# Kernel tuning notes

Measured on AMD Instinct MI355X. Metric: run time of the kernel, lower is better.

## Reference

```python
import jax, jax.numpy as jnp
import numpy as np

DIM = 1024
NUM_HEADS = 16
HEAD_DIM = DIM // NUM_HEADS
INNER_ITR = 4
INNER_LR = 1.0
SCALE_QKV = 1.0


def setup_inputs() -> dict:
    key = jax.random.key(0)
    k1, k2, k3 = jax.random.split(key, 3)
    B, N, C = 8, 1024, DIM
    x = jax.random.normal(k1, (B, N, C), dtype=jnp.float32)
    # Xavier-uniform-ish scaled dense kernels
    w_qkv = jax.random.normal(k2, (C, 3 * C), dtype=jnp.float32) * (1.0 / np.sqrt(C))
    w_proj = jax.random.normal(k3, (C, C), dtype=jnp.float32) * (1.0 / np.sqrt(C))
    b_proj = jnp.zeros((C,), dtype=jnp.float32)
    return {"x": x, "w_qkv": w_qkv, "w_proj": w_proj, "b_proj": b_proj, "training": 0}


def _mttt_base(q, k, v):
    """MTTT 'base' inner loop: per (B,H) linear model W,b trained by
    INNER_ITR full-batch GD steps on MSE reconstruction of v from k,
    then applied to q. Shapes: q,k,v are (B, H, N, d)."""
    B, H, N, d = q.shape
    W = jnp.zeros((B, H, d, d), dtype=q.dtype)
    b = jnp.zeros((B, H, 1, d), dtype=q.dtype)
    invN = 1.0 / N
    for _ in range(INNER_ITR):  # small fixed iteration count
        pred = jnp.einsum('bhnd,bhde->bhne', k, W) + b   # (B,H,N,d)
        err = pred - v
        gW = jnp.einsum('bhnd,bhne->bhde', k, err) * invN
        gb = jnp.mean(err, axis=2, keepdims=True)
        W = W - INNER_LR * gW
        b = b - INNER_LR * gb
    return jnp.einsum('bhnd,bhde->bhne', q, W) + b       # (B,H,N,d)


def reference(x, w_qkv, w_proj, b_proj, training):
    B, N, C = x.shape
    H, d = NUM_HEADS, HEAD_DIM
    qkv = jnp.einsum('bnc,ce->bne', x, w_qkv)            # (B,N,3C), qkv_bias=False
    qkv = qkv.reshape(B, N, 3, H, d).transpose(2, 0, 3, 1, 4)  # (3,B,H,N,d)
    qkv = qkv * SCALE_QKV
    q, k, v = qkv[0], qkv[1], qkv[2]
    # qk_norm=False -> identity; scale_q=False -> no q scaling
    out = _mttt_base(q, k, v)                            # (B,H,N,d)
    out = out.transpose(0, 2, 1, 3).reshape(B, N, C)
    out = jnp.einsum('bnc,cd->bnd', out, w_proj) + b_proj
    # proj dropout deterministic (training=False)
    return out
```

## Files before the change

### kernel.cpp

```cpp
#include <hip/hip_runtime.h>


#define SEQ    1024
#define NBATCH 8
#define DIMC   1024
#define NHEAD  16
#define HDIM   64
#define MROWS  8192
#define NQKV   3072

typedef __attribute__((ext_vector_type(8))) __bf16 bf16x8;
typedef __attribute__((ext_vector_type(4))) float  f32x4;

__device__ __forceinline__ unsigned short f2b(float f) {
  union { float f; unsigned int u; } v; v.f = f;
  unsigned int r = (v.u + 0x7FFFu + ((v.u >> 16) & 1u)) >> 16;
  return (unsigned short)r;
}

__device__ __forceinline__ void load_lds16(const void* g, void* l) {
  __builtin_amdgcn_global_load_lds(
      (__attribute__((address_space(1))) void*)(void*)(g),
      (__attribute__((address_space(3))) void*)(l), 16, 0, 0);
}

#define FENCE asm volatile("" ::: "memory")
#define BAR   __builtin_amdgcn_s_barrier()

__global__ __launch_bounds__(256) void prep(const float* __restrict__ x,
                                            const float* __restrict__ wq,
                                            const float* __restrict__ wp,
                                            unsigned short* __restrict__ xb,
                                            unsigned short* __restrict__ wqT,
                                            unsigned short* __restrict__ wpT) {
  __shared__ unsigned short tile[32][33];
  const int bid = blockIdx.x, tid = threadIdx.x;
  if (bid < 8192) {
    int i = bid * 256 + tid;
    float4 v = ((const float4*)x)[i];
    ushort4 o;
    o.x = f2b(v.x); o.y = f2b(v.y); o.z = f2b(v.z); o.w = f2b(v.w);
    ((ushort4*)xb)[i] = o;
    return;
  }
  const float* in; unsigned short* out; int R, Cc, tix;
  if (bid < 8192 + 3072) { tix = bid - 8192; in = wq; out = wqT; R = 1024; Cc = 3072; }
  else                   { tix = bid - 8192 - 3072; in = wp; out = wpT; R = 1024; Cc = 1024; }
  const int nbx = Cc / 32;
  const int c0 = (tix % nbx) * 32, r0 = (tix / nbx) * 32;
  const int tx = tid & 31, ty = tid >> 5;
  for (int i = ty; i < 32; i += 8)
    tile[i][tx] = f2b(in[(size_t)(r0 + i) * Cc + c0 + tx]);
  __syncthreads();
  for (int i = ty; i < 32; i += 8)
    out[(size_t)(c0 + i) * R + r0 + tx] = tile[tx][i];
}

template <int BM, int BN, int WM, int WN, int ASTRIDE, int BMODE, int PERB>
__device__ __forceinline__
void gemm_r3(const unsigned short* __restrict__ A,
             const unsigned short* __restrict__ BT,
             void* __restrict__ Cout,
             const float* __restrict__ bias,
             int N, int NBN) {
  constexpr int THREADS = WM * WN * 64;
  constexpr int MF      = BM / (WM * 16);
  constexpr int NF      = BN / (WN * 16);
  constexpr int TR      = THREADS / 4;
  constexpr int ABYTES  = BM * 64;
  constexpr int TBYTES  = (BM + BN) * 64;
  constexpr int CALLS   = TBYTES / (THREADS * 16);
  constexpr int NT      = 32;

  extern __shared__ __align__(16) char ldsb[];

  const int tid  = threadIdx.x;
  const int lane = tid & 63, wave = tid >> 6;
  const int wr = wave / WN, wc = wave % WN;
  const int frow = lane & 15, g4 = lane >> 4;
  const int cz = (g4 ^ ((frow >> 1) & 3)) * 16;

  const int cpx = gridDim.x >> 3;
  const int wg  = (blockIdx.x & 7) * cpx + (blockIdx.x >> 3);
  const int bm = wg / NBN, bn = wg % NBN;
  const size_t m0 = (size_t)bm * BM, n0 = (size_t)bn * BN;

  const unsigned short* BTb = PERB ? (BT + (m0 >> 10) * (size_t)(1024 * 1024)) : BT;

  const int trow = tid >> 2;
  const int scol = ((tid & 3) ^ ((tid >> 3) & 3)) * 8;
  const unsigned short* psrc[CALLS];
#pragma unroll
  for (int c = 0; c < CALLS; ++c) {
    const int rr = c * TR + trow;
    psrc[c] = (rr < BM) ? (A + (m0 + rr) * (size_t)ASTRIDE + scol)
                        : (BTb + (size_t)(n0 + rr - BM) * 1024 + scol);
  }

  f32x4 acc[MF][NF];
  if (BMODE == 2) {
    const float* bp = bias + (m0 >> 10) * (size_t)N;
#pragma unroll
    for (int j = 0; j < NF; ++j) {
      float4 bv = *(const float4*)&bp[n0 + wc * (BN / WN) + j * 16 + g4 * 4];
      f32x4 t; t[0] = bv.x; t[1] = bv.y; t[2] = bv.z; t[3] = bv.w;
#pragma unroll
      for (int i = 0; i < MF; ++i) acc[i][j] = t;
    }
  } else {
#pragma unroll
    for (int i = 0; i < MF; ++i)
#pragma unroll
      for (int j = 0; j < NF; ++j) acc[i][j] = f32x4{0.f, 0.f, 0.f, 0.f};
  }

  auto stage = [&](int tk, int buf) {
    char* base = ldsb + buf * TBYTES + wave * 1024;
#pragma unroll
    for (int c = 0; c < CALLS; ++c)
      load_lds16(psrc[c] + tk * 32, base + c * (THREADS * 16));
  };

  const int aoff = (wr * (BM / WM) + frow) * 64 + cz;
  const int boff = ABYTES + (wc * (BN / WN) + frow) * 64 + cz;

  stage(0, 0); stage(1, 1);
  asm volatile("s_waitcnt vmcnt(%0)" :: "i"(CALLS) : "memory");
  FENCE; BAR;

  int bcur = 0, bpre = 2;
#pragma unroll 1
  for (int t = 0; t < NT; ++t) {
    if (t + 2 < NT) stage(t + 2, bpre);
    const char* rb = ldsb + bcur * TBYTES;
    bf16x8 af[MF], bq[NF];
#pragma unroll
    for (int i = 0; i < MF; ++i) af[i] = *(const bf16x8*)(rb + aoff + i * 1024);
#pragma unroll
    for (int j = 0; j < NF; ++j) bq[j] = *(const bf16x8*)(rb + boff + j * 1024);
#pragma unroll
    for (int i = 0; i < MF; ++i)
#pragma unroll
      for (int j = 0; j < NF; ++j)
        acc[i][j] = __builtin_amdgcn_mfma_f32_16x16x32_bf16(bq[j], af[i],
                                                            acc[i][j], 0, 0, 0);
    if (t + 2 < NT) asm volatile("s_waitcnt vmcnt(%0)" :: "i"(CALLS) : "memory");
    else            asm volatile("s_waitcnt vmcnt(0)" ::: "memory");
    FENCE; BAR;
    bcur = (bcur == 2) ? 0 : bcur + 1;
    bpre = (bpre == 2) ? 0 : bpre + 1;
  }

  const size_t mbase = m0 + wr * (BM / WM) + frow;
  const size_t nbase = n0 + wc * (BN / WN) + g4 * 4;
  if (BMODE == 2) {
    float* C = (float*)Cout;
#pragma unroll
    for (int i = 0; i < MF; ++i)
#pragma unroll
      for (int j = 0; j < NF; ++j) {
        float4 o; o.x = acc[i][j][0]; o.y = acc[i][j][1];
        o.z = acc[i][j][2]; o.w = acc[i][j][3];
        *(float4*)&C[(mbase + i * 16) * N + nbase + j * 16] = o;
      }
  } else {
    unsigned short* C = (unsigned short*)Cout;
#pragma unroll
    for (int i = 0; i < MF; ++i)
#pragma unroll
      for (int j = 0; j < NF; ++j) {
        ushort4 o; o.x = f2b(acc[i][j][0]); o.y = f2b(acc[i][j][1]);
        o.z = f2b(acc[i][j][2]); o.w = f2b(acc[i][j][3]);
        *(ushort4*)&C[(mbase + i * 16) * N + nbase + j * 16] = o;
      }
  }
}

__global__ __launch_bounds__(512, 4) void g_qkv(const unsigned short* __restrict__ A,
                                                const unsigned short* __restrict__ BT,
                                                void* __restrict__ C,
                                                const float* __restrict__ bias, int N, int NBN) {
  gemm_r3<128, 256, 2, 4, 1024, 0, 0>(A, BT, C, bias, N, NBN);
}
__global__ __launch_bounds__(256, 3) void g_out(const unsigned short* __restrict__ A,
                                                const unsigned short* __restrict__ BT,
                                                void* __restrict__ C,
                                                const float* __restrict__ bias, int N, int NBN) {
  gemm_r3<128, 128, 2, 2, NQKV, 2, 1>(A, BT, C, bias, N, NBN);
}

__global__ __launch_bounds__(256) void stats_gd(const unsigned short* __restrict__ qkvb,
                                                unsigned short* __restrict__ Wfb,
                                                float* __restrict__ bvec) {
  __shared__ __align__(16) char smem[52224];
  unsigned short (*kd)[136] = (unsigned short(*)[136])(smem);
  unsigned short (*vd)[136] = (unsigned short(*)[136])(smem + 17408);
  unsigned short (*kn)[64]  = (unsigned short(*)[64])(smem + 34816);
  unsigned short (*vn)[64]  = (unsigned short(*)[64])(smem + 43008);
  float (*Gs)[68] = (float(*)[68])(smem);
  float (*Ps)[68] = (float(*)[68])(smem + 17408);
  float (*Ws)[68] = (float(*)[68])(smem + 34816);
  __shared__ float mks[64], mvs[64], bs[64];

  const int bh = blockIdx.x, b = bh >> 4, h = bh & 15;
  const int tid = threadIdx.x;
  const int lane = tid & 63, wave = tid >> 6;
  const int frow = lane & 15;
  const int fk = (lane >> 4) * 8;

  const unsigned short* kg = qkvb + (size_t)b * 1024 * 3072 + 1024 + h * 64;
  const unsigned short* vg = qkvb + (size_t)b * 1024 * 3072 + 2048 + h * 64;

  typedef __attribute__((ext_vector_type(8))) unsigned short u16x8;
  u16x8 onesu = {0x3F80, 0x3F80, 0x3F80, 0x3F80, 0x3F80, 0x3F80, 0x3F80, 0x3F80};
  const bf16x8 ones = __builtin_bit_cast(bf16x8, onesu);

  f32x4 accG[4], accP[4], accK1, accV1;
#pragma unroll
  for (int j = 0; j < 4; ++j) {
    accG[j] = f32x4{0.f, 0.f, 0.f, 0.f};
    accP[j] = f32x4{0.f, 0.f, 0.f, 0.f};
  }
  accK1 = f32x4{0.f, 0.f, 0.f, 0.f};
  accV1 = f32x4{0.f, 0.f, 0.f, 0.f};

  const size_t srcn = (size_t)(tid >> 3) * 3072 + (tid & 7) * 8;
  const int td = tid & 63, tng = tid >> 6;

  for (int ch = 0; ch < 16; ++ch) {
    const size_t nb0 = (size_t)ch * 64;
#pragma unroll
    for (int c = 0; c < 2; ++c) {
      load_lds16(kg + (nb0 + 32 * c) * 3072 + srcn, (char*)kn + c * 4096 + wave * 1024);
      load_lds16(vg + (nb0 + 32 * c) * 3072 + srcn, (char*)vn + c * 4096 + wave * 1024);
    }
    asm volatile("s_waitcnt vmcnt(0)" ::: "memory");
    FENCE; BAR;
    {
      alignas(16) unsigned short pk[16], pv[16];
#pragma unroll
      for (int j = 0; j < 16; ++j) {
        pk[j] = kn[tng * 16 + j][td];
        pv[j] = vn[tng * 16 + j][td];
      }
      *(uint4*)&kd[td][tng * 16]     = *(const uint4*)pk;
      *(uint4*)&kd[td][tng * 16 + 8] = *(const uint4*)(pk + 8);
      *(uint4*)&vd[td][tng * 16]     = *(const uint4*)pv;
      *(uint4*)&vd[td][tng * 16 + 8] = *(const uint4*)(pv + 8);
    }
    FENCE; BAR;
#pragma unroll
    for (int ks = 0; ks < 2; ++ks) {
      const int nb = ks * 32 + fk;
      bf16x8 afk = *(const bf16x8*)&kd[wave * 16 + frow][nb];
      bf16x8 afv = *(const bf16x8*)&vd[wave * 16 + frow][nb];
      bf16x8 kf[4], vf[4];
#pragma unroll
      for (int j = 0; j < 4; ++j) {
        kf[j] = *(const bf16x8*)&kd[j * 16 + frow][nb];
        vf[j] = *(const bf16x8*)&vd[j * 16 + frow][nb];
      }
#pragma unroll
      for (int j = 0; j < 4; ++j) {
        accG[j] = __builtin_amdgcn_mfma_f32_16x16x32_bf16(afk, kf[j], accG[j], 0, 0, 0);
        accP[j] = __builtin_amdgcn_mfma_f32_16x16x32_bf16(afk, vf[j], accP[j], 0, 0, 0);
      }
      accK1 = __builtin_amdgcn_mfma_f32_16x16x32_bf16(afk, ones, accK1, 0, 0, 0);
      accV1 = __builtin_amdgcn_mfma_f32_16x16x32_bf16(afv, ones, accV1, 0, 0, 0);
    }
    FENCE; BAR;
  }

  const float invN = 1.0f / (float)SEQ;
  const int orow = wave * 16 + (lane >> 4) * 4;
#pragma unroll
  for (int j = 0; j < 4; ++j)
#pragma unroll
    for (int r = 0; r < 4; ++r) {
      Gs[orow + r][j * 16 + frow] = accG[j][r] * invN;
      Ps[orow + r][j * 16 + frow] = accP[j][r] * invN;
    }
  if (frow == 0) {
#pragma unroll
    for (int r = 0; r < 4; ++r) {
      mks[orow + r] = accK1[r] * invN;
      mvs[orow + r] = accV1[r] * invN;
    }
  }
  const int r = tid >> 2;
  const int c0 = (tid & 3) * 16;
  if (tid < 64) bs[tid] = 0.f;
#pragma unroll
  for (int c = 0; c < 16; ++c) Ws[r][c0 + c] = 0.f;
  __syncthreads();

  for (int it = 0; it < 4; ++it) {
    float wn[16];
#pragma unroll
    for (int c = 0; c < 16; ++c)
      wn[c] = Ws[r][c0 + c] + Ps[r][c0 + c] - mks[r] * bs[c0 + c];
    for (int j = 0; j < 64; ++j) {
      float g = Gs[r][j];
#pragma unroll
      for (int c = 0; c < 16; ++c) wn[c] -= g * Ws[j][c0 + c];
    }
    float bn = 0.f;
    if (tid < 64) {
      bn = mvs[tid];
      for (int j = 0; j < 64; ++j) bn -= mks[j] * Ws[j][tid];
    }
    __syncthreads();
#pragma unroll
    for (int c = 0; c < 16; ++c) Ws[r][c0 + c] = wn[c];
    if (tid < 64) bs[tid] = bn;
    __syncthreads();
  }

  unsigned short* wout = Wfb + (size_t)bh * HDIM * HDIM;
#pragma unroll
  for (int c = 0; c < 16; ++c)
    wout[(size_t)r * HDIM + c0 + c] = f2b(Ws[r][c0 + c]);
  if (tid < 64) bvec[(size_t)bh * HDIM + tid] = bs[tid];
}

__global__ __launch_bounds__(256) void wc_build(const unsigned short* __restrict__ wpT,
                                                const unsigned short* __restrict__ Wfb,
                                                unsigned short* __restrict__ WcT,
                                                const float* __restrict__ wp,
                                                const float* __restrict__ bvec,
                                                float* __restrict__ part) {
  const int tid = threadIdx.x;
  if (blockIdx.y == 4) {
    if (blockIdx.x >= 64) return;
    const int p  = (blockIdx.x & 3) * 256 + tid;
    const int cc = blockIdx.x >> 2;
    float s[8];
#pragma unroll
    for (int b = 0; b < 8; ++b) s[b] = 0.f;
    const int c0 = cc * 64;
    for (int c = c0; c < c0 + 64; ++c) {
      float w = wp[(size_t)c * 1024 + p];
#pragma unroll
      for (int b = 0; b < 8; ++b) s[b] += bvec[b * 1024 + c] * w;
    }
    float* dst = part + (size_t)cc * 8192;
#pragma unroll
    for (int b = 0; b < 8; ++b) dst[b * 1024 + p] = s[b];
    return;
  }
  const int bh = blockIdx.x;
  const int pblk = blockIdx.y;
  const int b = bh >> 4, h = bh & 15;
  const int lane = tid & 63, wave = tid >> 6;
  const int frow = lane & 15, g4 = lane >> 4, fk = g4 * 8;
  const int p0 = pblk * 256 + wave * 64;

  f32x4 acc[4][4];
#pragma unroll
  for (int i = 0; i < 4; ++i)
#pragma unroll
    for (int j = 0; j < 4; ++j) acc[i][j] = f32x4{0.f, 0.f, 0.f, 0.f};

  const unsigned short* wb = Wfb + (size_t)bh * 4096;
#pragma unroll
  for (int kk = 0; kk < 2; ++kk) {
    bf16x8 af[4], bq[4];
#pragma unroll
    for (int i = 0; i < 4; ++i)
      af[i] = *(const bf16x8*)&wpT[(size_t)(p0 + i * 16 + frow) * 1024 + h * 64 + kk * 32 + fk];
#pragma unroll
    for (int j = 0; j < 4; ++j)
      bq[j] = *(const bf16x8*)&wb[(size_t)(j * 16 + frow) * 64 + kk * 32 + fk];
#pragma unroll
    for (int i = 0; i < 4; ++i)
#pragma unroll
      for (int j = 0; j < 4; ++j)
        acc[i][j] = __builtin_amdgcn_mfma_f32_16x16x32_bf16(bq[j], af[i], acc[i][j], 0, 0, 0);
  }

  unsigned short* dst = WcT + (size_t)b * 1024 * 1024;
#pragma unroll
  for (int i = 0; i < 4; ++i)
#pragma unroll
    for (int j = 0; j < 4; ++j) {
      ushort4 o; o.x = f2b(acc[i][j][0]); o.y = f2b(acc[i][j][1]);
      o.z = f2b(acc[i][j][2]); o.w = f2b(acc[i][j][3]);
      *(ushort4*)&dst[(size_t)(p0 + i * 16 + frow) * 1024 + h * 64 + j * 16 + g4 * 4] = o;
    }
}

__global__ __launch_bounds__(256) void bc_reduce(const float* __restrict__ part,
                                                 const float* __restrict__ b_proj,
                                                 float* __restrict__ bc) {
  const int idx = blockIdx.x * 256 + threadIdx.x;
  const int p = idx & 1023;
  float s = b_proj[p];
#pragma unroll
  for (int cc = 0; cc < 16; ++cc) s += part[(size_t)cc * 8192 + idx];
  bc[idx] = s;
}

extern "C" void kernel_launch(void* const* d_in, const int* in_sizes, int n_in,
                              void* d_out, int out_size, void* d_ws, size_t ws_size,
                              hipStream_t stream) {
  const float* x      = (const float*)d_in[0];
  const float* w_qkv  = (const float*)d_in[1];
  const float* w_proj = (const float*)d_in[2];
  const float* b_proj = (const float*)d_in[3];

  char* ws = (char*)d_ws;
  unsigned short* xb    = (unsigned short*)(ws + 0);
  unsigned short* wqT   = (unsigned short*)(ws + 16777216);
  unsigned short* wpT   = (unsigned short*)(ws + 23068672);
  unsigned short* qkvb  = (unsigned short*)(ws + 25165824);
  unsigned short* WcT   = (unsigned short*)(ws + 109051904);
  unsigned short* Wfb   = (unsigned short*)(ws + 125829120);
  float*          bvec  = (float*)(ws + 126877696);
  float*          bc    = (float*)(ws + 126910464);
  float*          bpart = (float*)(ws + 126943232);
  if (ws_size < (size_t)127467520) return;

  hipFuncSetAttribute((const void*)g_qkv, hipFuncAttributeMaxDynamicSharedMemorySize, 73728);
  hipFuncSetAttribute((const void*)g_out, hipFuncAttributeMaxDynamicSharedMemorySize, 49152);

  prep<<<dim3(8192 + 3072 + 1024), 256, 0, stream>>>(x, w_qkv, w_proj, xb, wqT, wpT);
  g_qkv<<<dim3(768), dim3(512), 73728, stream>>>(xb, wqT, qkvb, nullptr, NQKV, 12);
  stats_gd<<<128, 256, 0, stream>>>(qkvb, Wfb, bvec);
  wc_build<<<dim3(128, 5), 256, 0, stream>>>(wpT, Wfb, WcT, w_proj, bvec, bpart);
  bc_reduce<<<32, 256, 0, stream>>>(bpart, b_proj, bc);
  g_out<<<dim3(512), dim3(256), 49152, stream>>>(qkvb, WcT, d_out, bc, DIMC, 8);
}
```

Measured before the change: 166.1 us.

## Split per-head statistics reduction across two blocks and add separate GD solve kernel

The fused stats+GD kernel, which ran only 128 blocks, is split in two. A statistics kernel now uses 256 blocks, each reducing half the sequence and writing raw MFMA accumulators to workspace that reuses the xb region. A new gd_solve kernel sums the two partials and runs the inner gradient-descent iterations. The aim is better CU occupancy during the memory-bound Gram-matrix pass, at the cost of one extra launch and a partial-sum round trip through global memory.

```diff
diff --git a/kernel.cpp b/kernel.cpp
--- a/kernel.cpp
+++ b/kernel.cpp
@@ -189,20 +189,17 @@
   gemm_r3<128, 128, 2, 2, NQKV, 2, 1>(A, BT, C, bias, N, NBN);
 }
 
-__global__ __launch_bounds__(256) void stats_gd(const unsigned short* __restrict__ qkvb,
-                                                unsigned short* __restrict__ Wfb,
-                                                float* __restrict__ bvec) {
-  __shared__ __align__(16) char smem[52224];
+__global__ __launch_bounds__(256) void stats_part(const unsigned short* __restrict__ qkvb,
+                                                  float* __restrict__ spart) {
+  __shared__ __align__(16) char smem[51200];
   unsigned short (*kd)[136] = (unsigned short(*)[136])(smem);
   unsigned short (*vd)[136] = (unsigned short(*)[136])(smem + 17408);
   unsigned short (*kn)[64]  = (unsigned short(*)[64])(smem + 34816);
   unsigned short (*vn)[64]  = (unsigned short(*)[64])(smem + 43008);
-  float (*Gs)[68] = (float(*)[68])(smem);
-  float (*Ps)[68] = (float(*)[68])(smem + 17408);
-  float (*Ws)[68] = (float(*)[68])(smem + 34816);
-  __shared__ float mks[64], mvs[64], bs[64];
-
-  const int bh = blockIdx.x, b = bh >> 4, h = bh & 15;
+
+  const int bh2 = blockIdx.x;
+  const int bh = bh2 >> 1, half = bh2 & 1;
+  const int b = bh >> 4, h = bh & 15;
   const int tid = threadIdx.x;
   const int lane = tid & 63, wave = tid >> 6;
   const int frow = lane & 15;
@@ -227,8 +224,8 @@
   const size_t srcn = (size_t)(tid >> 3) * 3072 + (tid & 7) * 8;
   const int td = tid & 63, tng = tid >> 6;
 
-  for (int ch = 0; ch < 16; ++ch) {
-    const size_t nb0 = (size_t)ch * 64;
+  for (int ch = 0; ch < 8; ++ch) {
+    const size_t nb0 = (size_t)half * 512 + (size_t)ch * 64;
 #pragma unroll
     for (int c = 0; c < 2; ++c) {
       load_lds16(kg + (nb0 + 32 * c) * 3072 + srcn, (char*)kn + c * 4096 + wave * 1024);
@@ -271,20 +268,54 @@
     FENCE; BAR;
   }
 
+  float* dst = spart + (size_t)bh2 * 40 * 256;
+#pragma unroll
+  for (int j = 0; j < 4; ++j)
+#pragma unroll
+    for (int r = 0; r < 4; ++r) dst[(j * 4 + r) * 256 + tid] = accG[j][r];
+#pragma unroll
+  for (int j = 0; j < 4; ++j)
+#pragma unroll
+    for (int r = 0; r < 4; ++r) dst[(16 + j * 4 + r) * 256 + tid] = accP[j][r];
+#pragma unroll
+  for (int r = 0; r < 4; ++r) dst[(32 + r) * 256 + tid] = accK1[r];
+#pragma unroll
+  for (int r = 0; r < 4; ++r) dst[(36 + r) * 256 + tid] = accV1[r];
+}
+
+__global__ __launch_bounds__(256) void gd_solve(const float* __restrict__ spart,
+                                                unsigned short* __restrict__ Wfb,
+                                                float* __restrict__ bvec) {
+  __shared__ float Gs[64][68];
+  __shared__ float Ps[64][68];
+  __shared__ float Ws[64][68];
+  __shared__ float mks[64], mvs[64], bs[64];
+
+  const int bh = blockIdx.x;
+  const int tid = threadIdx.x;
+  const int lane = tid & 63, wave = tid >> 6;
+  const int frow = lane & 15;
+
+  const float* s0 = spart + (size_t)(bh * 2) * 40 * 256;
+  const float* s1 = spart + (size_t)(bh * 2 + 1) * 40 * 256;
+  float fsum[40];
+#pragma unroll
+  for (int w = 0; w < 40; ++w) fsum[w] = s0[w * 256 + tid] + s1[w * 256 + tid];
+
   const float invN = 1.0f / (float)SEQ;
   const int orow = wave * 16 + (lane >> 4) * 4;
 #pragma unroll
   for (int j = 0; j < 4; ++j)
 #pragma unroll
     for (int r = 0; r < 4; ++r) {
-      Gs[orow + r][j * 16 + frow] = accG[j][r] * invN;
-      Ps[orow + r][j * 16 + frow] = accP[j][r] * invN;
+      Gs[orow + r][j * 16 + frow] = fsum[j * 4 + r] * invN;
+      Ps[orow + r][j * 16 + frow] = fsum[16 + j * 4 + r] * invN;
     }
   if (frow == 0) {
 #pragma unroll
     for (int r = 0; r < 4; ++r) {
-      mks[orow + r] = accK1[r] * invN;
-      mvs[orow + r] = accV1[r] * invN;
+      mks[orow + r] = fsum[32 + r] * invN;
+      mvs[orow + r] = fsum[36 + r] * invN;
     }
   }
   const int r = tid >> 2;
@@ -410,6 +441,7 @@
 
   char* ws = (char*)d_ws;
   unsigned short* xb    = (unsigned short*)(ws + 0);
+  float*          spart = (float*)(ws + 0);
   unsigned short* wqT   = (unsigned short*)(ws + 16777216);
   unsigned short* wpT   = (unsigned short*)(ws + 23068672);
   unsigned short* qkvb  = (unsigned short*)(ws + 25165824);
@@ -425,7 +457,8 @@
 
   prep<<<dim3(8192 + 3072 + 1024), 256, 0, stream>>>(x, w_qkv, w_proj, xb, wqT, wpT);
   g_qkv<<<dim3(768), dim3(512), 73728, stream>>>(xb, wqT, qkvb, nullptr, NQKV, 12);
-  stats_gd<<<128, 256, 0, stream>>>(qkvb, Wfb, bvec);
+  stats_part<<<256, 256, 0, stream>>>(qkvb, spart);
+  gd_solve<<<128, 256, 0, stream>>>(spart, Wfb, bvec);
   wc_build<<<dim3(128, 5), 256, 0, stream>>>(wpT, Wfb, WcT, w_proj, bvec, bpart);
   bc_reduce<<<32, 256, 0, stream>>>(bpart, b_proj, bc);
   g_out<<<dim3(512), dim3(256), 49152, stream>>>(qkvb, WcT, d_out, bc, DIMC, 8);
```

Measured after the change: 163.2 us, median of 8. About the same (-1.7%).
